# Kernel optimization log

Hardware: AMD Instinct MI355X
Metric: run time of the kernel (lower is better)

The kernel has to match this reference:

```python
import jax, jax.numpy as jnp
import numpy as np
from jax import lax

B, R, F = 100, 15, 4096       # batch, regions, feature dim
V, E, D, A, T = 10000, 1024, 1024, 512, 500  # vocab, embed, decoder, attention, topic
LIN = 1024                    # autoencoder linear output width
NT = 5                        # sentences per paragraph
L = 52                        # max caption length


def setup_inputs() -> dict:
    key = jax.random.key(0)
    ks = jax.random.split(key, 16)
    g = lambda i, shp, s: jax.random.normal(ks[i], shp, jnp.float32) * s
    return {
        "image_features": g(0, (B, R, F), 1.0),
        "encoded_captions": jax.random.randint(ks[1], (B, NT, L), 0, V),
        "caption_lengths": jax.random.randint(ks[2], (B, NT), 1, L),
        # autoencoder
        "W_lt": g(3, (LIN, F), 0.02), "b_lt": jnp.zeros((LIN,), jnp.float32),
        "conv_w": g(4, (6, 1, 15, 26), 0.05), "conv_b": jnp.zeros((6,), jnp.float32),
        # attention MLP (weight_norm linears == plain linears mathematically)
        "W_feat": g(5, (A, F), 0.02), "b_feat": jnp.zeros((A,), jnp.float32),
        "W_dec": g(6, (A, D), 0.02), "b_dec": jnp.zeros((A,), jnp.float32),
        "W_top": g(7, (A, T), 0.02), "b_top": jnp.zeros((A,), jnp.float32),
        "W_full": g(8, (1, A), 0.02), "b_full": jnp.zeros((1,), jnp.float32),
        # embedding + LSTM cells + output heads
        "emb": g(9, (V, E), 0.1),
        "W_ih1": g(10, (4 * D, E + F + D), 0.01), "W_hh1": g(11, (4 * D, D), 0.01),
        "b_ih1": jnp.zeros((4 * D,), jnp.float32), "b_hh1": jnp.zeros((4 * D,), jnp.float32),
        "W_ih2": g(12, (4 * D, F + D), 0.01), "W_hh2": g(13, (4 * D, D), 0.01),
        "b_ih2": jnp.zeros((4 * D,), jnp.float32), "b_hh2": jnp.zeros((4 * D,), jnp.float32),
        "W_fc1": g(14, (V, D), 0.02), "b_fc1": jnp.zeros((V,), jnp.float32),
        "W_fc": g(15, (V, D), 0.02), "b_fc": jnp.zeros((V,), jnp.float32),
    }


def _lstm_cell(x, h, c, W_ih, W_hh, b_ih, b_hh):
    gates = x @ W_ih.T + b_ih + h @ W_hh.T + b_hh
    i, f, g_, o = jnp.split(gates, 4, axis=-1)
    c = jax.nn.sigmoid(f) * c + jax.nn.sigmoid(i) * jnp.tanh(g_)
    h = jax.nn.sigmoid(o) * jnp.tanh(c)
    return h, c


def reference(image_features, encoded_captions, caption_lengths, W_lt, b_lt,
              conv_w, conv_b, W_feat, b_feat, W_dec, b_dec, W_top, b_top,
              W_full, b_full, emb, W_ih1, W_hh1, b_ih1, b_hh1,
              W_ih2, W_hh2, b_ih2, b_hh2, W_fc1, b_fc1, W_fc, b_fc):
    def per_sample(img, caps, lens):
        # img (R,F), caps (NT,L) int, lens (NT,) int
        img_mean = img.mean(0)  # (F,)
        # autoencoder: linear 4096->1024, conv2d(1->6, k=(15,26), stride 2)
        x = (img @ W_lt.T + b_lt)[None, None]  # (1,1,R,LIN)
        conv = lax.conv_general_dilated(x, conv_w, (2, 2), "VALID",
                                        dimension_numbers=("NCHW", "OIHW", "NCHW"))
        topics = conv[0, :, 0, :] + conv_b[:, None]  # (6, T=500)
        att1 = img @ W_feat.T + b_feat               # (R,A), precomputed once
        # last word of each sentence: caps[t, lens[t]-1]
        last_words = jnp.take_along_axis(caps, (lens - 1)[:, None], axis=1)[:, 0]  # (NT,)
        last_embs = emb[last_words]                  # (NT,E)

        def step(carry, tup):
            h1, c1, h2, c2 = carry
            topic_t, emb_t = tup
            # top-down attention LSTM: cat([h2, img_mean, word_emb])
            x1 = jnp.concatenate([h2, img_mean, emb_t])
            h1, c1 = _lstm_cell(x1, h1, c1, W_ih1, W_hh1, b_ih1, b_hh1)
            # attention over R regions (dropout is identity in eval)
            att = jax.nn.relu(att1 + (h1 @ W_dec.T + b_dec) + (topic_t @ W_top.T + b_top))
            scores = att @ W_full[0] + b_full[0]     # (R,)
            alpha = jax.nn.softmax(scores)
            awe = alpha @ img                        # (F,)
            preds1 = h1 @ W_fc1.T + b_fc1            # (V,)
            h2, c2 = _lstm_cell(jnp.concatenate([awe, h1]), h2, c2,
                                W_ih2, W_hh2, b_ih2, b_hh2)
            preds = h2 @ W_fc.T + b_fc               # (V,)
            return (h1, c1, h2, c2), (preds, preds1)

        z = jnp.zeros((D,), img.dtype)
        _, (preds, preds1) = lax.scan(step, (z, z, z, z), (topics[:NT], last_embs))
        return preds, preds1                          # (NT,V) each

    preds, preds1 = jax.vmap(per_sample)(image_features, encoded_captions, caption_lengths)
    return preds, preds1, encoded_captions, caption_lengths - 1
```

## Files before the change

### kernel.cpp

```cpp
#include <hip/hip_runtime.h>

typedef __attribute__((ext_vector_type(8))) short short8;
typedef __attribute__((ext_vector_type(4))) short short4v;
typedef __attribute__((ext_vector_type(4))) float f32x4;

__device__ __forceinline__ unsigned short f2bf(float f) {
  unsigned int u = __float_as_uint(f);
  u += 0x7fffu + ((u >> 16) & 1u);
  return (unsigned short)(u >> 16);
}
__device__ __forceinline__ float bf2f(unsigned short u) {
  return __uint_as_float(((unsigned int)u) << 16);
}
__device__ __forceinline__ float sigm(float x) { return 1.f / (1.f + expf(-x)); }

template<int NKC>
__global__ __launch_bounds__(256) void gemm_v5(
    const unsigned short* __restrict__ X, int ldx,
    const unsigned short* __restrict__ W, int ldw, int N,
    unsigned short* __restrict__ C, long long slotStride)
{
  __shared__ short8 lds[3584];
  const int tid = threadIdx.x;
  const int lane = tid & 63, wv = tid >> 6;
  const int l16 = lane & 15, kg = (lane >> 4) * 8;
  const int mbase = blockIdx.y * 112;
  const int ncol = blockIdx.x * 64 + wv * 16 + l16;
  const int nrow = (ncol < N) ? ncol : (N - 1);
  const long long k0 = (long long)blockIdx.z * (NKC * 256);
  C += (long long)blockIdx.z * slotStride;

  const unsigned short* wp = W + (size_t)nrow * ldw + kg + k0;
  const unsigned short* xb = X + (size_t)(mbase + l16) * ldx + kg + k0;
  const size_t xrow = (size_t)16 * ldx;

  f32x4 acc[7];
#pragma unroll
  for (int i = 0; i < 7; ++i) acc[i] = (f32x4){0.f, 0.f, 0.f, 0.f};

  for (int kc = 0; kc < NKC; ++kc) {
    if (kc) __syncthreads();
    short8 wbuf[8];
#pragma unroll
    for (int ks = 0; ks < 8; ++ks)
      wbuf[ks] = *(const short8*)(wp + kc * 256 + ks * 32);
    short8 xst[14];
#pragma unroll
    for (int i = 0; i < 14; ++i) {
      const int f = wv + i * 4, mt = f >> 3, ks = f & 7;
      xst[i] = *(const short8*)(xb + (size_t)mt * xrow + kc * 256 + ks * 32);
    }
#pragma unroll
    for (int i = 0; i < 14; ++i) lds[(wv + i * 4) * 64 + lane] = xst[i];
    __syncthreads();
#pragma unroll
    for (int ks = 0; ks < 8; ++ks)
#pragma unroll
      for (int mt = 0; mt < 7; ++mt) {
        short8 a = lds[(mt * 8 + ks) * 64 + lane];
        acc[mt] = __builtin_amdgcn_mfma_f32_16x16x32_bf16(a, wbuf[ks], acc[mt], 0, 0, 0);
      }
  }
  if (ncol < N) {
    const int r0 = (lane >> 4) * 4;
#pragma unroll
    for (int mt = 0; mt < 7; ++mt)
#pragma unroll
      for (int r = 0; r < 4; ++r)
        C[(size_t)(mbase + mt * 16 + r0 + r) * N + ncol] = f2bf(acc[mt][r]);
  }
}

template<int NKC>
__global__ __launch_bounds__(256) void gemm_v5f(
    const unsigned short* __restrict__ X, int ldx,
    const float* __restrict__ W, int ldw, int N,
    unsigned short* __restrict__ C, long long slotStride)
{
  __shared__ short8 lds[3584];
  const int tid = threadIdx.x;
  const int lane = tid & 63, wv = tid >> 6;
  const int l16 = lane & 15, kg = (lane >> 4) * 8;
  const int mbase = blockIdx.y * 112;
  const int ncol = blockIdx.x * 64 + wv * 16 + l16;
  const int nrow = (ncol < N) ? ncol : (N - 1);
  const long long k0 = (long long)blockIdx.z * (NKC * 256);
  C += (long long)blockIdx.z * slotStride;

  const float* wp = W + (size_t)nrow * ldw + kg + k0;
  const unsigned short* xb = X + (size_t)(mbase + l16) * ldx + kg + k0;
  const size_t xrow = (size_t)16 * ldx;

  f32x4 acc[7];
#pragma unroll
  for (int i = 0; i < 7; ++i) acc[i] = (f32x4){0.f, 0.f, 0.f, 0.f};

  for (int kc = 0; kc < NKC; ++kc) {
    if (kc) __syncthreads();
    float4 wa[8], wb[8];
#pragma unroll
    for (int ks = 0; ks < 8; ++ks) {
      wa[ks] = *(const float4*)(wp + kc * 256 + ks * 32);
      wb[ks] = *(const float4*)(wp + kc * 256 + ks * 32 + 4);
    }
    short8 xst[14];
#pragma unroll
    for (int i = 0; i < 14; ++i) {
      const int f = wv + i * 4, mt = f >> 3, ks = f & 7;
      xst[i] = *(const short8*)(xb + (size_t)mt * xrow + kc * 256 + ks * 32);
    }
#pragma unroll
    for (int i = 0; i < 14; ++i) lds[(wv + i * 4) * 64 + lane] = xst[i];
    __syncthreads();
#pragma unroll
    for (int ks = 0; ks < 8; ++ks) {
      short8 w;
      w[0] = (short)f2bf(wa[ks].x); w[1] = (short)f2bf(wa[ks].y);
      w[2] = (short)f2bf(wa[ks].z); w[3] = (short)f2bf(wa[ks].w);
      w[4] = (short)f2bf(wb[ks].x); w[5] = (short)f2bf(wb[ks].y);
      w[6] = (short)f2bf(wb[ks].z); w[7] = (short)f2bf(wb[ks].w);
#pragma unroll
      for (int mt = 0; mt < 7; ++mt) {
        short8 a = lds[(mt * 8 + ks) * 64 + lane];
        acc[mt] = __builtin_amdgcn_mfma_f32_16x16x32_bf16(a, w, acc[mt], 0, 0, 0);
      }
    }
  }
  if (ncol < N) {
    const int r0 = (lane >> 4) * 4;
#pragma unroll
    for (int mt = 0; mt < 7; ++mt)
#pragma unroll
      for (int r = 0; r < 4; ++r)
        C[(size_t)(mbase + mt * 16 + r0 + r) * N + ncol] = f2bf(acc[mt][r]);
  }
}

__global__ __launch_bounds__(256) void k_cvt4(const float* __restrict__ src,
                                              unsigned short* __restrict__ dst, int n4) {
  int i = blockIdx.x * 256 + threadIdx.x;
  if (i >= n4) return;
  float4 v = ((const float4*)src)[i];
  short4v o; o[0] = (short)f2bf(v.x); o[1] = (short)f2bf(v.y);
  o[2] = (short)f2bf(v.z); o[3] = (short)f2bf(v.w);
  ((short4v*)dst)[i] = o;
}

__global__ __launch_bounds__(256) void k_pack_g1(const float* __restrict__ Wih1,
    const float* __restrict__ Whh1, unsigned short* __restrict__ Wg1) {
  int i = blockIdx.x * 256 + threadIdx.x;
  if (i >= 4096 * 512) return;
  int row = i >> 9, c4 = i & 511;
  const float* src = (c4 < 256) ? Wih1 + (size_t)row * 6144 + c4 * 4
                                : Whh1 + (size_t)row * 1024 + (c4 - 256) * 4;
  float4 v = *(const float4*)src;
  short4v o; o[0] = (short)f2bf(v.x); o[1] = (short)f2bf(v.y);
  o[2] = (short)f2bf(v.z); o[3] = (short)f2bf(v.w);
  ((short4v*)Wg1)[i] = o;
}

__global__ __launch_bounds__(256) void k_pack_g2(const float* __restrict__ Wih2,
    const float* __restrict__ Whh2, unsigned short* __restrict__ Wg2) {
  int i = blockIdx.x * 256 + threadIdx.x;
  if (i >= 4096 * 1536) return;
  int row = i / 1536, c4 = i - row * 1536;
  const float* src = (c4 < 1280) ? Wih2 + (size_t)row * 5120 + c4 * 4
                                 : Whh2 + (size_t)row * 1024 + (c4 - 1280) * 4;
  float4 v = *(const float4*)src;
  short4v o; o[0] = (short)f2bf(v.x); o[1] = (short)f2bf(v.y);
  o[2] = (short)f2bf(v.z); o[3] = (short)f2bf(v.w);
  ((short4v*)Wg2)[i] = o;
}

__global__ __launch_bounds__(256) void k_ximg(const float* __restrict__ src,
                                              unsigned short* __restrict__ dst) {
  int idx = blockIdx.x * 256 + threadIdx.x;
  int row = idx >> 12;
  dst[idx] = (row < 1500) ? f2bf(src[idx]) : (unsigned short)0;
}

__global__ __launch_bounds__(256) void k_mean(const float* __restrict__ img,
                                              unsigned short* __restrict__ dst) {
  int idx = blockIdx.x * 256 + threadIdx.x;
  int b = idx >> 12, f = idx & 4095;
  unsigned short r = 0;
  if (b < 100) {
    float s = 0.f;
    for (int rr = 0; rr < 15; ++rr) s += img[((size_t)b * 15 + rr) * 4096 + f];
    r = f2bf(s * (1.f / 15.f));
  }
  dst[idx] = r;
}

__global__ __launch_bounds__(256) void k_reduce(const unsigned short* __restrict__ P,
    long long ss, int nslots, const float* __restrict__ bias, int colmask,
    float* __restrict__ out, int total) {
  int idx = blockIdx.x * 256 + threadIdx.x;
  if (idx >= total) return;
  float s = bias ? bias[idx & colmask] : 0.f;
  for (int sl = 0; sl < nslots; ++sl) s += bf2f(P[(size_t)sl * ss + idx]);
  out[idx] = s;
}

__global__ __launch_bounds__(512) void k_conv(const float* __restrict__ lin,
    const float* __restrict__ cw, const float* __restrict__ cb,
    float* __restrict__ topics) {
  int b = blockIdx.x;
  __shared__ float L[15 * 1024];
  for (int i = threadIdx.x; i < 15 * 1024; i += 512) L[i] = lin[(size_t)b * 15360 + i];
  __syncthreads();
  for (int idx = threadIdx.x; idx < 2500; idx += 512) {
    int tt = idx / 500, w = idx - tt * 500;
    float s = cb[tt];
    for (int kh = 0; kh < 15; ++kh) {
      const float* lr = &L[kh * 1024 + 2 * w];
      const float* wr = &cw[(tt * 15 + kh) * 26];
#pragma unroll
      for (int kw = 0; kw < 26; ++kw) s += lr[kw] * wr[kw];
    }
    topics[(size_t)b * 2500 + idx] = s;
  }
}

__global__ __launch_bounds__(256) void k_ttop(const float* __restrict__ topics,
    const float* __restrict__ Wt, const float* __restrict__ btp,
    float* __restrict__ ttop) {
  int idx = blockIdx.x * 256 + threadIdx.x;
  int r = idx >> 9, n = idx & 511;
  const float4* tr = (const float4*)(topics + (size_t)r * 500);
  const float4* wr = (const float4*)(Wt + (size_t)n * 500);
  float s = btp[n];
  for (int k = 0; k < 125; ++k) {
    float4 a = tr[k], w = wr[k];
    s += a.x * w.x + a.y * w.y + a.z * w.z + a.w * w.w;
  }
  ttop[idx] = s;
}

__global__ void k_words(const int* __restrict__ caps, const int* __restrict__ lens,
                        int* __restrict__ words, float* __restrict__ out3) {
  int idx = blockIdx.x * 256 + threadIdx.x;
  if (idx >= 500) return;
  int len = lens[idx];
  words[idx] = caps[idx * 52 + len - 1];
  out3[idx] = (float)(len - 1);
}

__global__ void k_caps(const int* __restrict__ caps, float* __restrict__ out2) {
  int idx = blockIdx.x * 256 + threadIdx.x;
  if (idx < 26000) out2[idx] = (float)caps[idx];
}

__global__ __launch_bounds__(256) void k_gather(const float* __restrict__ emb,
    const int* __restrict__ words, unsigned short* __restrict__ Xemb) {
  int idx = blockIdx.x * 256 + threadIdx.x;
  int bt = idx >> 10, e = idx & 1023;
  Xemb[idx] = (bt < 500) ? f2bf(emb[(size_t)words[bt] * 1024 + e]) : (unsigned short)0;
}

__global__ __launch_bounds__(256) void k_gbase1(const unsigned short* __restrict__ P,
    const float* __restrict__ bih, const float* __restrict__ bhh,
    float* __restrict__ gb) {
  int idx = blockIdx.x * 256 + threadIdx.x;
  int m = idx >> 12, n = idx & 4095;
  float s = bih[n] + bhh[n];
#pragma unroll
  for (int sl = 0; sl < 8; ++sl) s += bf2f(P[((size_t)sl * 112 + m) * 4096 + n]);
  gb[idx] = s;
}

__global__ __launch_bounds__(256) void k_lstm1(const unsigned short* __restrict__ P,
    const float* __restrict__ gb1, const float* __restrict__ gemb, int t,
    float* __restrict__ c1, unsigned short* __restrict__ Xh1,
    unsigned short* __restrict__ X1, unsigned short* __restrict__ X2) {
  int idx = blockIdx.x * 256 + threadIdx.x;
  int b = idx >> 10, j = idx & 1023;
  float g[4];
#pragma unroll
  for (int x = 0; x < 4; ++x) {
    int col = (x << 10) + j;
    float s = gb1[b * 4096 + col] + gemb[((size_t)b * 5 + t) * 4096 + col];
#pragma unroll
    for (int sl = 0; sl < 8; ++sl) s += bf2f(P[((size_t)sl * 112 + b) * 4096 + col]);
    g[x] = s;
  }
  float c = sigm(g[1]) * c1[idx] + sigm(g[0]) * tanhf(g[2]);
  float h = sigm(g[3]) * tanhf(c);
  c1[idx] = c;
  unsigned short hb = f2bf(h);
  Xh1[idx] = hb;
  X1[b * 2048 + 1024 + j] = hb;
  X2[(size_t)b * 6144 + 4096 + j] = hb;
}

__global__ __launch_bounds__(256) void k_att(const float* __restrict__ att1,
    const unsigned short* __restrict__ padec, const float* __restrict__ bdec,
    const float* __restrict__ ttop, const float* __restrict__ wfull,
    const float* __restrict__ bfull, int t, float* __restrict__ scores) {
  int wid = (blockIdx.x * 256 + threadIdx.x) >> 6;
  int lane = threadIdx.x & 63;
  if (wid >= 1500) return;
  int b = wid / 15;
  const float* a1 = att1 + (size_t)wid * 512;
  const float* tp = ttop + ((size_t)b * 5 + t) * 512;
  float s = 0.f;
#pragma unroll
  for (int j = 0; j < 8; ++j) {
    int n = lane * 8 + j;
    float ad = bdec[n] + bf2f(padec[(size_t)b * 512 + n])
             + bf2f(padec[(size_t)(112 + b) * 512 + n])
             + bf2f(padec[(size_t)(224 + b) * 512 + n])
             + bf2f(padec[(size_t)(336 + b) * 512 + n]);
    float v = a1[n] + ad + tp[n];
    s += fmaxf(v, 0.f) * wfull[n];
  }
#pragma unroll
  for (int o = 32; o; o >>= 1) s += __shfl_down(s, o, 64);
  if (lane == 0) scores[wid] = s + bfull[0];
}

__global__ __launch_bounds__(256) void k_softawe(const float* __restrict__ scores,
    const unsigned short* __restrict__ Ximg, unsigned short* __restrict__ X2) {
  int b = blockIdx.x;
  __shared__ float al[16];
  if (threadIdx.x == 0) {
    float m = -1e30f;
    for (int r = 0; r < 15; ++r) m = fmaxf(m, scores[b * 15 + r]);
    float e[15]; float sum = 0.f;
    for (int r = 0; r < 15; ++r) { e[r] = expf(scores[b * 15 + r] - m); sum += e[r]; }
    float inv = 1.f / sum;
    for (int r = 0; r < 15; ++r) al[r] = e[r] * inv;
  }
  __syncthreads();
  for (int f = threadIdx.x; f < 4096; f += 256) {
    float s = 0.f;
#pragma unroll
    for (int r = 0; r < 15; ++r) s += al[r] * bf2f(Ximg[((size_t)b * 15 + r) * 4096 + f]);
    X2[(size_t)b * 6144 + f] = f2bf(s);
  }
}

__global__ __launch_bounds__(256) void k_lstm2(const unsigned short* __restrict__ P,
    const float* __restrict__ bih, const float* __restrict__ bhh,
    float* __restrict__ c2, unsigned short* __restrict__ Xh2,
    unsigned short* __restrict__ X1, unsigned short* __restrict__ X2) {
  int idx = blockIdx.x * 256 + threadIdx.x;
  int b = idx >> 10, j = idx & 1023;
  float g[4];
#pragma unroll
  for (int x = 0; x < 4; ++x) {
    int col = (x << 10) + j;
    float s = bih[col] + bhh[col];
#pragma unroll
    for (int sl = 0; sl < 12; ++sl) s += bf2f(P[((size_t)sl * 112 + b) * 4096 + col]);
    g[x] = s;
  }
  float c = sigm(g[1]) * c2[idx] + sigm(g[0]) * tanhf(g[2]);
  float h = sigm(g[3]) * tanhf(c);
  c2[idx] = c;
  unsigned short hb = f2bf(h);
  Xh2[idx] = hb;
  X1[b * 2048 + j] = hb;
  X2[(size_t)b * 6144 + 5120 + j] = hb;
}

__global__ __launch_bounds__(256) void k_eppred(const unsigned short* __restrict__ P,
    const float* __restrict__ bias, float* __restrict__ outp, int t) {
  int idx = blockIdx.x * 256 + threadIdx.x;
  if (idx >= 1000000) return;
  int b = idx / 10000, v = idx - b * 10000;
  outp[((size_t)b * 5 + t) * 10000 + v] = bias[v]
      + bf2f(P[(size_t)b * 10000 + v])         + bf2f(P[(size_t)(112 + b) * 10000 + v])
      + bf2f(P[(size_t)(224 + b) * 10000 + v]) + bf2f(P[(size_t)(336 + b) * 10000 + v]);
}

extern "C" void kernel_launch(void* const* d_in, const int* in_sizes, int n_in,
                              void* d_out, int out_size, void* d_ws, size_t ws_size,
                              hipStream_t stream) {
  (void)in_sizes; (void)n_in; (void)out_size;
  const float* imgf  = (const float*)d_in[0];
  const int*   caps  = (const int*)d_in[1];
  const int*   lens  = (const int*)d_in[2];
  const float* W_lt  = (const float*)d_in[3];
  const float* b_lt  = (const float*)d_in[4];
  const float* convw = (const float*)d_in[5];
  const float* convb = (const float*)d_in[6];
  const float* W_feat = (const float*)d_in[7];
  const float* b_feat = (const float*)d_in[8];
  const float* W_dec = (const float*)d_in[9];
  const float* b_dec = (const float*)d_in[10];
  const float* W_top = (const float*)d_in[11];
  const float* b_top = (const float*)d_in[12];
  const float* W_full = (const float*)d_in[13];
  const float* b_full = (const float*)d_in[14];
  const float* emb   = (const float*)d_in[15];
  const float* W_ih1 = (const float*)d_in[16];
  const float* W_hh1 = (const float*)d_in[17];
  const float* b_ih1 = (const float*)d_in[18];
  const float* b_hh1 = (const float*)d_in[19];
  const float* W_ih2 = (const float*)d_in[20];
  const float* W_hh2 = (const float*)d_in[21];
  const float* b_ih2 = (const float*)d_in[22];
  const float* b_hh2 = (const float*)d_in[23];
  const float* W_fc1 = (const float*)d_in[24];
  const float* b_fc1 = (const float*)d_in[25];
  const float* W_fc  = (const float*)d_in[26];
  const float* b_fc  = (const float*)d_in[27];
  float* out = (float*)d_out;

  char* ws = (char*)d_ws;
  size_t off = 0;
  auto alloc = [&](size_t bytes) -> size_t {
    size_t o = off; off = (off + bytes + 255) & ~(size_t)255; return o;
  };
  const size_t oXimg  = alloc(1568ull * 4096 * 2);
  const size_t oXmean = alloc(112ull * 4096 * 2);
  const size_t oXemb  = alloc(560ull * 1024 * 2);
  const size_t oZERO  = off;
  const size_t oX1    = alloc(112ull * 2048 * 2);
  const size_t oX2    = alloc(112ull * 6144 * 2);
  const size_t oXh1   = alloc(112ull * 1024 * 2);
  const size_t oXh2   = alloc(112ull * 1024 * 2);
  const size_t oc1    = alloc(100ull * 1024 * 4);
  const size_t oc2    = alloc(100ull * 1024 * 4);
  const size_t zeroBytes = off - oZERO;
  const size_t olin   = alloc(1568ull * 1024 * 4);
  const size_t otop   = alloc(100ull * 2500 * 4);
  const size_t ottop  = alloc(500ull * 512 * 4);
  const size_t oatt1  = alloc(1568ull * 512 * 4);
  const size_t oscore = alloc(1536ull * 4);
  const size_t ogb1   = alloc(112ull * 4096 * 4);
  const size_t ogemb  = alloc(560ull * 4096 * 4);
  const size_t owords = alloc(512ull * 4);
  const size_t opg    = alloc(12ull * 112 * 4096 * 2);
  const size_t opx    = alloc(4ull * 1568 * 1024 * 2);
  const size_t oWg1   = alloc(4096ull * 2048 * 2);
  const size_t oWg2   = alloc(4096ull * 6144 * 2);
  const size_t oWfc1b = alloc(10000ull * 1024 * 2);
  const size_t oWfcb  = alloc(10000ull * 1024 * 2);
  const size_t oWdecb = alloc(512ull * 1024 * 2);
  const size_t oWltb  = alloc(1024ull * 4096 * 2);
  const size_t oWftb  = alloc(512ull * 4096 * 2);
  if (ws_size < off) return;

  unsigned short* Ximg  = (unsigned short*)(ws + oXimg);
  unsigned short* Xmean = (unsigned short*)(ws + oXmean);
  unsigned short* Xemb  = (unsigned short*)(ws + oXemb);
  unsigned short* X1    = (unsigned short*)(ws + oX1);
  unsigned short* X2    = (unsigned short*)(ws + oX2);
  unsigned short* Xh1   = (unsigned short*)(ws + oXh1);
  unsigned short* Xh2   = (unsigned short*)(ws + oXh2);
  float* c1    = (float*)(ws + oc1);
  float* c2    = (float*)(ws + oc2);
  float* lin   = (float*)(ws + olin);
  float* topics = (float*)(ws + otop);
  float* ttop  = (float*)(ws + ottop);
  float* att1  = (float*)(ws + oatt1);
  float* score = (float*)(ws + oscore);
  float* gb1   = (float*)(ws + ogb1);
  float* gemb  = (float*)(ws + ogemb);
  int*   words = (int*)(ws + owords);
  unsigned short* pg = (unsigned short*)(ws + opg);
  unsigned short* px = (unsigned short*)(ws + opx);
  unsigned short* Wg1   = (unsigned short*)(ws + oWg1);
  unsigned short* Wg2   = (unsigned short*)(ws + oWg2);
  unsigned short* Wfc1b = (unsigned short*)(ws + oWfc1b);
  unsigned short* Wfcb  = (unsigned short*)(ws + oWfcb);
  unsigned short* Wdecb = (unsigned short*)(ws + oWdecb);
  unsigned short* Wltb  = (unsigned short*)(ws + oWltb);
  unsigned short* Wftb  = (unsigned short*)(ws + oWftb);

  const long long S4 = 112ll * 4096;
  const long long SA = 112ll * 512;
  const long long SP = 112ll * 10000;

  hipMemsetAsync(ws + oZERO, 0, zeroBytes, stream);

  k_ximg<<<25088, 256, 0, stream>>>(imgf, Ximg);
  k_mean<<<1792, 256, 0, stream>>>(imgf, Xmean);
  k_pack_g1<<<8192, 256, 0, stream>>>(W_ih1, W_hh1, Wg1);
  k_pack_g2<<<24576, 256, 0, stream>>>(W_ih2, W_hh2, Wg2);
  k_cvt4<<<10000, 256, 0, stream>>>(W_fc1, Wfc1b, 2560000);
  k_cvt4<<<10000, 256, 0, stream>>>(W_fc, Wfcb, 2560000);
  k_cvt4<<<512, 256, 0, stream>>>(W_dec, Wdecb, 131072);
  k_cvt4<<<4096, 256, 0, stream>>>(W_lt, Wltb, 1048576);
  k_cvt4<<<2048, 256, 0, stream>>>(W_feat, Wftb, 524288);
  gemm_v5<4><<<dim3(16, 14, 4), 256, 0, stream>>>(Ximg, 4096, Wltb, 4096, 1024,
                                                  px, 1568ll * 1024);
  k_reduce<<<6272, 256, 0, stream>>>(px, 1568ll * 1024, 4, b_lt, 1023, lin, 1568 * 1024);
  k_conv<<<100, 512, 0, stream>>>(lin, convw, convb, topics);
  k_ttop<<<1000, 256, 0, stream>>>(topics, W_top, b_top, ttop);
  gemm_v5<4><<<dim3(8, 14, 4), 256, 0, stream>>>(Ximg, 4096, Wftb, 4096, 512,
                                                 px, 1568ll * 512);
  k_reduce<<<3136, 256, 0, stream>>>(px, 1568ll * 512, 4, b_feat, 511, att1, 1568 * 512);
  k_words<<<2, 256, 0, stream>>>(caps, lens, words, out + 10026000);
  k_caps<<<102, 256, 0, stream>>>(caps, out + 10000000);
  k_gather<<<2240, 256, 0, stream>>>(emb, words, Xemb);
  gemm_v5f<2><<<dim3(64, 1, 8), 256, 0, stream>>>(Xmean, 4096, W_ih1 + 1024, 6144, 4096,
                                                  pg, S4);
  k_gbase1<<<1792, 256, 0, stream>>>(pg, b_ih1, b_hh1, gb1);
  gemm_v5f<1><<<dim3(64, 5, 4), 256, 0, stream>>>(Xemb, 1024, W_ih1 + 5120, 6144, 4096,
                                                  px, 560ll * 4096);
  k_reduce<<<8960, 256, 0, stream>>>(px, 560ll * 4096, 4, nullptr, 4095, gemb, 560 * 4096);

  for (int t = 0; t < 5; ++t) {
    gemm_v5<1><<<dim3(64, 1, 8), 256, 0, stream>>>(X1, 2048, Wg1, 2048, 4096, pg, S4);
    k_lstm1<<<400, 256, 0, stream>>>(pg, gb1, gemb, t, c1, Xh1, X1, X2);
    gemm_v5<1><<<dim3(8, 1, 4), 256, 0, stream>>>(Xh1, 1024, Wdecb, 1024, 512, px, SA);
    k_att<<<375, 256, 0, stream>>>(att1, px, b_dec, ttop, W_full, b_full, t, score);
    k_softawe<<<100, 256, 0, stream>>>(score, Ximg, X2);
    gemm_v5<1><<<dim3(157, 1, 4), 256, 0, stream>>>(Xh1, 1024, Wfc1b, 1024, 10000, px, SP);
    k_eppred<<<3907, 256, 0, stream>>>(px, b_fc1, out + 5000000, t);
    gemm_v5<2><<<dim3(64, 1, 12), 256, 0, stream>>>(X2, 6144, Wg2, 6144, 4096, pg, S4);
    k_lstm2<<<400, 256, 0, stream>>>(pg, b_ih2, b_hh2, c2, Xh2, X1, X2);
    gemm_v5<1><<<dim3(157, 1, 4), 256, 0, stream>>>(Xh2, 1024, Wfcb, 1024, 10000, px, SP);
    k_eppred<<<3907, 256, 0, stream>>>(px, b_fc, out, t);
  }
}
```

Measured before the change: 789.7 us.

## Fuse weight packing, attention, and fc1/dec GEMMs; reduce launch count

Result: faster. 704.5 us (-10.8%).

```diff
diff --git a/kernel.cpp b/kernel.cpp
--- a/kernel.cpp
+++ b/kernel.cpp
@@ -136,40 +136,46 @@
   }
 }
 
-__global__ __launch_bounds__(256) void k_cvt4(const float* __restrict__ src,
-                                              unsigned short* __restrict__ dst, int n4) {
+__global__ __launch_bounds__(256) void k_pack_all(
+    const float* __restrict__ Wih1, const float* __restrict__ Whh1,
+    const float* __restrict__ Wih2, const float* __restrict__ Whh2,
+    const float* __restrict__ Wfc1, const float* __restrict__ Wdec,
+    const float* __restrict__ Wfc,  const float* __restrict__ Wlt,
+    const float* __restrict__ Wft,  const float* __restrict__ Wtop,
+    unsigned short* __restrict__ Wg1, unsigned short* __restrict__ Wg2,
+    unsigned short* __restrict__ Wcat, unsigned short* __restrict__ Wfcb,
+    unsigned short* __restrict__ Wltb, unsigned short* __restrict__ Wftb,
+    unsigned short* __restrict__ Wtopb)
+{
   int i = blockIdx.x * 256 + threadIdx.x;
-  if (i >= n4) return;
-  float4 v = ((const float4*)src)[i];
+  float4 v; unsigned short* dst; long long di;
+  if (i < 2097152) {
+    int row = i >> 9, c4 = i & 511;
+    const float* s = (c4 < 256) ? Wih1 + (size_t)row * 6144 + c4 * 4
+                                : Whh1 + (size_t)row * 1024 + (c4 - 256) * 4;
+    v = *(const float4*)s; dst = Wg1; di = i;
+  } else if (i < 8388608) {
+    int j = i - 2097152; int row = j / 1536, c4 = j - row * 1536;
+    const float* s = (c4 < 1280) ? Wih2 + (size_t)row * 5120 + c4 * 4
+                                 : Whh2 + (size_t)row * 1024 + (c4 - 1280) * 4;
+    v = *(const float4*)s; dst = Wg2; di = j;
+  } else if (i < 11079680) {
+    int j = i - 8388608; int row = j >> 8, c4 = j & 255;
+    const float* s = (row < 10000) ? Wfc1 + (size_t)row * 1024 + c4 * 4
+                                   : Wdec + (size_t)(row - 10000) * 1024 + c4 * 4;
+    v = *(const float4*)s; dst = Wcat; di = j;
+  } else if (i < 13639680) { int j = i - 11079680; v = ((const float4*)Wfc)[j]; dst = Wfcb; di = j; }
+  else if (i < 14688256) { int j = i - 13639680; v = ((const float4*)Wlt)[j]; dst = Wltb; di = j; }
+  else if (i < 15212544) { int j = i - 14688256; v = ((const float4*)Wft)[j]; dst = Wftb; di = j; }
+  else {
+    int j = i - 15212544; int n = j >> 7, c4 = j & 127;
+    v = (c4 < 125) ? *(const float4*)(Wtop + (size_t)n * 500 + c4 * 4)
+                   : (float4){0.f, 0.f, 0.f, 0.f};
+    dst = Wtopb; di = j;
+  }
   short4v o; o[0] = (short)f2bf(v.x); o[1] = (short)f2bf(v.y);
   o[2] = (short)f2bf(v.z); o[3] = (short)f2bf(v.w);
-  ((short4v*)dst)[i] = o;
-}
-
-__global__ __launch_bounds__(256) void k_pack_g1(const float* __restrict__ Wih1,
-    const float* __restrict__ Whh1, unsigned short* __restrict__ Wg1) {
-  int i = blockIdx.x * 256 + threadIdx.x;
-  if (i >= 4096 * 512) return;
-  int row = i >> 9, c4 = i & 511;
-  const float* src = (c4 < 256) ? Wih1 + (size_t)row * 6144 + c4 * 4
-                                : Whh1 + (size_t)row * 1024 + (c4 - 256) * 4;
-  float4 v = *(const float4*)src;
-  short4v o; o[0] = (short)f2bf(v.x); o[1] = (short)f2bf(v.y);
-  o[2] = (short)f2bf(v.z); o[3] = (short)f2bf(v.w);
-  ((short4v*)Wg1)[i] = o;
-}
-
-__global__ __launch_bounds__(256) void k_pack_g2(const float* __restrict__ Wih2,
-    const float* __restrict__ Whh2, unsigned short* __restrict__ Wg2) {
-  int i = blockIdx.x * 256 + threadIdx.x;
-  if (i >= 4096 * 1536) return;
-  int row = i / 1536, c4 = i - row * 1536;
-  const float* src = (c4 < 1280) ? Wih2 + (size_t)row * 5120 + c4 * 4
-                                 : Whh2 + (size_t)row * 1024 + (c4 - 1280) * 4;
-  float4 v = *(const float4*)src;
-  short4v o; o[0] = (short)f2bf(v.x); o[1] = (short)f2bf(v.y);
-  o[2] = (short)f2bf(v.z); o[3] = (short)f2bf(v.w);
-  ((short4v*)Wg2)[i] = o;
+  ((short4v*)dst)[di] = o;
 }
 
 __global__ __launch_bounds__(256) void k_ximg(const float* __restrict__ src,
@@ -202,12 +208,18 @@
   out[idx] = s;
 }
 
-__global__ __launch_bounds__(512) void k_conv(const float* __restrict__ lin,
-    const float* __restrict__ cw, const float* __restrict__ cb,
-    float* __restrict__ topics) {
+__global__ __launch_bounds__(512) void k_conv(const unsigned short* __restrict__ px,
+    const float* __restrict__ blt, const float* __restrict__ cw,
+    const float* __restrict__ cb, float* __restrict__ topics) {
   int b = blockIdx.x;
   __shared__ float L[15 * 1024];
-  for (int i = threadIdx.x; i < 15 * 1024; i += 512) L[i] = lin[(size_t)b * 15360 + i];
+  for (int i = threadIdx.x; i < 15 * 1024; i += 512) {
+    float s = blt[i & 1023];
+#pragma unroll
+    for (int sl = 0; sl < 4; ++sl)
+      s += bf2f(px[(size_t)sl * 1605632 + (size_t)b * 15360 + i]);
+    L[i] = s;
+  }
   __syncthreads();
   for (int idx = threadIdx.x; idx < 2500; idx += 512) {
     int tt = idx / 500, w = idx - tt * 500;
@@ -222,33 +234,24 @@
   }
 }
 
-__global__ __launch_bounds__(256) void k_ttop(const float* __restrict__ topics,
-    const float* __restrict__ Wt, const float* __restrict__ btp,
-    float* __restrict__ ttop) {
-  int idx = blockIdx.x * 256 + threadIdx.x;
-  int r = idx >> 9, n = idx & 511;
-  const float4* tr = (const float4*)(topics + (size_t)r * 500);
-  const float4* wr = (const float4*)(Wt + (size_t)n * 500);
-  float s = btp[n];
-  for (int k = 0; k < 125; ++k) {
-    float4 a = tr[k], w = wr[k];
-    s += a.x * w.x + a.y * w.y + a.z * w.z + a.w * w.w;
-  }
-  ttop[idx] = s;
-}
-
-__global__ void k_words(const int* __restrict__ caps, const int* __restrict__ lens,
-                        int* __restrict__ words, float* __restrict__ out3) {
-  int idx = blockIdx.x * 256 + threadIdx.x;
-  if (idx >= 500) return;
-  int len = lens[idx];
-  words[idx] = caps[idx * 52 + len - 1];
-  out3[idx] = (float)(len - 1);
-}
-
-__global__ void k_caps(const int* __restrict__ caps, float* __restrict__ out2) {
+__global__ __launch_bounds__(256) void k_padtop(const float* __restrict__ topics,
+    unsigned short* __restrict__ Xtop) {
+  int idx = blockIdx.x * 256 + threadIdx.x;
+  if (idx >= 560 * 512) return;
+  int r = idx >> 9, k = idx & 511;
+  Xtop[idx] = (r < 500 && k < 500) ? f2bf(topics[(size_t)r * 500 + k]) : (unsigned short)0;
+}
+
+__global__ void k_wc(const int* __restrict__ caps, const int* __restrict__ lens,
+                     int* __restrict__ words, float* __restrict__ out2,
+                     float* __restrict__ out3) {
   int idx = blockIdx.x * 256 + threadIdx.x;
   if (idx < 26000) out2[idx] = (float)caps[idx];
+  if (idx < 500) {
+    int len = lens[idx];
+    words[idx] = caps[idx * 52 + len - 1];
+    out3[idx] = (float)(len - 1);
+  }
 }
 
 __global__ __launch_bounds__(256) void k_gather(const float* __restrict__ emb,
@@ -293,50 +296,54 @@
   X2[(size_t)b * 6144 + 4096 + j] = hb;
 }
 
-__global__ __launch_bounds__(256) void k_att(const float* __restrict__ att1,
+__global__ __launch_bounds__(256) void k_attawe(const float* __restrict__ att1,
     const unsigned short* __restrict__ padec, const float* __restrict__ bdec,
-    const float* __restrict__ ttop, const float* __restrict__ wfull,
-    const float* __restrict__ bfull, int t, float* __restrict__ scores) {
-  int wid = (blockIdx.x * 256 + threadIdx.x) >> 6;
-  int lane = threadIdx.x & 63;
-  if (wid >= 1500) return;
-  int b = wid / 15;
-  const float* a1 = att1 + (size_t)wid * 512;
-  const float* tp = ttop + ((size_t)b * 5 + t) * 512;
-  float s = 0.f;
-#pragma unroll
-  for (int j = 0; j < 8; ++j) {
-    int n = lane * 8 + j;
-    float ad = bdec[n] + bf2f(padec[(size_t)b * 512 + n])
-             + bf2f(padec[(size_t)(112 + b) * 512 + n])
-             + bf2f(padec[(size_t)(224 + b) * 512 + n])
-             + bf2f(padec[(size_t)(336 + b) * 512 + n]);
-    float v = a1[n] + ad + tp[n];
-    s += fmaxf(v, 0.f) * wfull[n];
-  }
-#pragma unroll
-  for (int o = 32; o; o >>= 1) s += __shfl_down(s, o, 64);
-  if (lane == 0) scores[wid] = s + bfull[0];
-}
-
-__global__ __launch_bounds__(256) void k_softawe(const float* __restrict__ scores,
+    const float* __restrict__ btop, const unsigned short* __restrict__ ttopb,
+    const float* __restrict__ wfull, int t,
     const unsigned short* __restrict__ Ximg, unsigned short* __restrict__ X2) {
   int b = blockIdx.x;
+  int tid = threadIdx.x;
+  int r = tid & 15, ch = tid >> 4;
+  __shared__ float sp[16][17];
   __shared__ float al[16];
-  if (threadIdx.x == 0) {
+  float s = 0.f;
+  if (r < 15) {
+    const float* a1 = att1 + ((size_t)b * 15 + r) * 512;
+    const unsigned short* tp = ttopb + ((size_t)b * 5 + t) * 512;
+#pragma unroll
+    for (int j = 0; j < 32; ++j) {
+      int n = ch * 32 + j;
+      float ad = bdec[n] + btop[n]
+               + bf2f(padec[((size_t)0 * 112 + b) * 10512 + 10000 + n])
+               + bf2f(padec[((size_t)1 * 112 + b) * 10512 + 10000 + n])
+               + bf2f(padec[((size_t)2 * 112 + b) * 10512 + 10000 + n])
+               + bf2f(padec[((size_t)3 * 112 + b) * 10512 + 10000 + n]);
+      float v = a1[n] + ad + bf2f(tp[n]);
+      s += fmaxf(v, 0.f) * wfull[n];
+    }
+  }
+  sp[r][ch] = s;
+  __syncthreads();
+  if (tid == 0) {
+    float sc[15];
     float m = -1e30f;
-    for (int r = 0; r < 15; ++r) m = fmaxf(m, scores[b * 15 + r]);
-    float e[15]; float sum = 0.f;
-    for (int r = 0; r < 15; ++r) { e[r] = expf(scores[b * 15 + r] - m); sum += e[r]; }
+    for (int rr = 0; rr < 15; ++rr) {
+      float x = 0.f;
+      for (int cc = 0; cc < 16; ++cc) x += sp[rr][cc];
+      sc[rr] = x; m = fmaxf(m, x);
+    }
+    float sum = 0.f;
+    for (int rr = 0; rr < 15; ++rr) { sc[rr] = expf(sc[rr] - m); sum += sc[rr]; }
     float inv = 1.f / sum;
-    for (int r = 0; r < 15; ++r) al[r] = e[r] * inv;
+    for (int rr = 0; rr < 15; ++rr) al[rr] = sc[rr] * inv;
   }
   __syncthreads();
-  for (int f = threadIdx.x; f < 4096; f += 256) {
-    float s = 0.f;
-#pragma unroll
-    for (int r = 0; r < 15; ++r) s += al[r] * bf2f(Ximg[((size_t)b * 15 + r) * 4096 + f]);
-    X2[(size_t)b * 6144 + f] = f2bf(s);
+  for (int f = tid; f < 4096; f += 256) {
+    float s2 = 0.f;
+#pragma unroll
+    for (int rr = 0; rr < 15; ++rr)
+      s2 += al[rr] * bf2f(Ximg[((size_t)b * 15 + rr) * 4096 + f]);
+    X2[(size_t)b * 6144 + f] = f2bf(s2);
   }
 }
 
@@ -365,13 +372,13 @@
 }
 
 __global__ __launch_bounds__(256) void k_eppred(const unsigned short* __restrict__ P,
-    const float* __restrict__ bias, float* __restrict__ outp, int t) {
+    const float* __restrict__ bias, float* __restrict__ outp, int t, int ldp) {
   int idx = blockIdx.x * 256 + threadIdx.x;
   if (idx >= 1000000) return;
   int b = idx / 10000, v = idx - b * 10000;
   outp[((size_t)b * 5 + t) * 10000 + v] = bias[v]
-      + bf2f(P[(size_t)b * 10000 + v])         + bf2f(P[(size_t)(112 + b) * 10000 + v])
-      + bf2f(P[(size_t)(224 + b) * 10000 + v]) + bf2f(P[(size_t)(336 + b) * 10000 + v]);
+      + bf2f(P[(size_t)(0 * 112 + b) * ldp + v]) + bf2f(P[(size_t)(112 + b) * ldp + v])
+      + bf2f(P[(size_t)(224 + b) * ldp + v])     + bf2f(P[(size_t)(336 + b) * ldp + v]);
 }
 
 extern "C" void kernel_launch(void* const* d_in, const int* in_sizes, int n_in,
@@ -392,7 +399,7 @@
   const float* W_top = (const float*)d_in[11];
   const float* b_top = (const float*)d_in[12];
   const float* W_full = (const float*)d_in[13];
-  const float* b_full = (const float*)d_in[14];
+  const float* b_full = (const float*)d_in[14];  (void)b_full;
   const float* emb   = (const float*)d_in[15];
   const float* W_ih1 = (const float*)d_in[16];
   const float* W_hh1 = (const float*)d_in[17];
@@ -424,23 +431,22 @@
   const size_t oc1    = alloc(100ull * 1024 * 4);
   const size_t oc2    = alloc(100ull * 1024 * 4);
   const size_t zeroBytes = off - oZERO;
-  const size_t olin   = alloc(1568ull * 1024 * 4);
   const size_t otop   = alloc(100ull * 2500 * 4);
-  const size_t ottop  = alloc(500ull * 512 * 4);
+  const size_t oXtop  = alloc(560ull * 512 * 2);
+  const size_t oTtopb = alloc(560ull * 512 * 2);
   const size_t oatt1  = alloc(1568ull * 512 * 4);
-  const size_t oscore = alloc(1536ull * 4);
   const size_t ogb1   = alloc(112ull * 4096 * 4);
   const size_t ogemb  = alloc(560ull * 4096 * 4);
   const size_t owords = alloc(512ull * 4);
   const size_t opg    = alloc(12ull * 112 * 4096 * 2);
-  const size_t opx    = alloc(4ull * 1568 * 1024 * 2);
+  const size_t opx    = alloc(4ull * 560 * 4096 * 2);
   const size_t oWg1   = alloc(4096ull * 2048 * 2);
   const size_t oWg2   = alloc(4096ull * 6144 * 2);
-  const size_t oWfc1b = alloc(10000ull * 1024 * 2);
+  const size_t oWcat  = alloc(10512ull * 1024 * 2);
   const size_t oWfcb  = alloc(10000ull * 1024 * 2);
-  const size_t oWdecb = alloc(512ull * 1024 * 2);
   const size_t oWltb  = alloc(1024ull * 4096 * 2);
   const size_t oWftb  = alloc(512ull * 4096 * 2);
+  const size_t oWtopb = alloc(512ull * 512 * 2);
   if (ws_size < off) return;
 
   unsigned short* Ximg  = (unsigned short*)(ws + oXimg);
@@ -452,11 +458,10 @@
   unsigned short* Xh2   = (unsigned short*)(ws + oXh2);
   float* c1    = (float*)(ws + oc1);
   float* c2    = (float*)(ws + oc2);
-  float* lin   = (float*)(ws + olin);
   float* topics = (float*)(ws + otop);
-  float* ttop  = (float*)(ws + ottop);
+  unsigned short* Xtop  = (unsigned short*)(ws + oXtop);
+  unsigned short* Ttopb = (unsigned short*)(ws + oTtopb);
   float* att1  = (float*)(ws + oatt1);
-  float* score = (float*)(ws + oscore);
   float* gb1   = (float*)(ws + ogb1);
   float* gemb  = (float*)(ws + ogemb);
   int*   words = (int*)(ws + owords);
@@ -464,37 +469,32 @@
   unsigned short* px = (unsigned short*)(ws + opx);
   unsigned short* Wg1   = (unsigned short*)(ws + oWg1);
   unsigned short* Wg2   = (unsigned short*)(ws + oWg2);
-  unsigned short* Wfc1b = (unsigned short*)(ws + oWfc1b);
+  unsigned short* Wcat  = (unsigned short*)(ws + oWcat);
   unsigned short* Wfcb  = (unsigned short*)(ws + oWfcb);
-  unsigned short* Wdecb = (unsigned short*)(ws + oWdecb);
   unsigned short* Wltb  = (unsigned short*)(ws + oWltb);
   unsigned short* Wftb  = (unsigned short*)(ws + oWftb);
-
-  const long long S4 = 112ll * 4096;
-  const long long SA = 112ll * 512;
-  const long long SP = 112ll * 10000;
+  unsigned short* Wtopb = (unsigned short*)(ws + oWtopb);
+
+  const long long S4  = 112ll * 4096;
+  const long long SP1 = 112ll * 10512;
+  const long long SP  = 112ll * 10000;
 
   hipMemsetAsync(ws + oZERO, 0, zeroBytes, stream);
 
   k_ximg<<<25088, 256, 0, stream>>>(imgf, Ximg);
   k_mean<<<1792, 256, 0, stream>>>(imgf, Xmean);
-  k_pack_g1<<<8192, 256, 0, stream>>>(W_ih1, W_hh1, Wg1);
-  k_pack_g2<<<24576, 256, 0, stream>>>(W_ih2, W_hh2, Wg2);
-  k_cvt4<<<10000, 256, 0, stream>>>(W_fc1, Wfc1b, 2560000);
-  k_cvt4<<<10000, 256, 0, stream>>>(W_fc, Wfcb, 2560000);
-  k_cvt4<<<512, 256, 0, stream>>>(W_dec, Wdecb, 131072);
-  k_cvt4<<<4096, 256, 0, stream>>>(W_lt, Wltb, 1048576);
-  k_cvt4<<<2048, 256, 0, stream>>>(W_feat, Wftb, 524288);
+  k_pack_all<<<59680, 256, 0, stream>>>(W_ih1, W_hh1, W_ih2, W_hh2, W_fc1, W_dec,
+                                        W_fc, W_lt, W_feat, W_top,
+                                        Wg1, Wg2, Wcat, Wfcb, Wltb, Wftb, Wtopb);
   gemm_v5<4><<<dim3(16, 14, 4), 256, 0, stream>>>(Ximg, 4096, Wltb, 4096, 1024,
                                                   px, 1568ll * 1024);
-  k_reduce<<<6272, 256, 0, stream>>>(px, 1568ll * 1024, 4, b_lt, 1023, lin, 1568 * 1024);
-  k_conv<<<100, 512, 0, stream>>>(lin, convw, convb, topics);
-  k_ttop<<<1000, 256, 0, stream>>>(topics, W_top, b_top, ttop);
+  k_conv<<<100, 512, 0, stream>>>(px, b_lt, convw, convb, topics);
+  k_padtop<<<1120, 256, 0, stream>>>(topics, Xtop);
+  gemm_v5<2><<<dim3(8, 5, 1), 256, 0, stream>>>(Xtop, 512, Wtopb, 512, 512, Ttopb, 0);
   gemm_v5<4><<<dim3(8, 14, 4), 256, 0, stream>>>(Ximg, 4096, Wftb, 4096, 512,
                                                  px, 1568ll * 512);
   k_reduce<<<3136, 256, 0, stream>>>(px, 1568ll * 512, 4, b_feat, 511, att1, 1568 * 512);
-  k_words<<<2, 256, 0, stream>>>(caps, lens, words, out + 10026000);
-  k_caps<<<102, 256, 0, stream>>>(caps, out + 10000000);
+  k_wc<<<102, 256, 0, stream>>>(caps, lens, words, out + 10000000, out + 10026000);
   k_gather<<<2240, 256, 0, stream>>>(emb, words, Xemb);
   gemm_v5f<2><<<dim3(64, 1, 8), 256, 0, stream>>>(Xmean, 4096, W_ih1 + 1024, 6144, 4096,
                                                   pg, S4);
@@ -506,14 +506,12 @@
   for (int t = 0; t < 5; ++t) {
     gemm_v5<1><<<dim3(64, 1, 8), 256, 0, stream>>>(X1, 2048, Wg1, 2048, 4096, pg, S4);
     k_lstm1<<<400, 256, 0, stream>>>(pg, gb1, gemb, t, c1, Xh1, X1, X2);
-    gemm_v5<1><<<dim3(8, 1, 4), 256, 0, stream>>>(Xh1, 1024, Wdecb, 1024, 512, px, SA);
-    k_att<<<375, 256, 0, stream>>>(att1, px, b_dec, ttop, W_full, b_full, t, score);
-    k_softawe<<<100, 256, 0, stream>>>(score, Ximg, X2);
-    gemm_v5<1><<<dim3(157, 1, 4), 256, 0, stream>>>(Xh1, 1024, Wfc1b, 1024, 10000, px, SP);
-    k_eppred<<<3907, 256, 0, stream>>>(px, b_fc1, out + 5000000, t);
+    gemm_v5<1><<<dim3(165, 1, 4), 256, 0, stream>>>(Xh1, 1024, Wcat, 1024, 10512, px, SP1);
+    k_attawe<<<100, 256, 0, stream>>>(att1, px, b_dec, b_top, Ttopb, W_full, t, Ximg, X2);
+    k_eppred<<<3907, 256, 0, stream>>>(px, b_fc1, out + 5000000, t, 10512);
     gemm_v5<2><<<dim3(64, 1, 12), 256, 0, stream>>>(X2, 6144, Wg2, 6144, 4096, pg, S4);
     k_lstm2<<<400, 256, 0, stream>>>(pg, b_ih2, b_hh2, c2, Xh2, X1, X2);
     gemm_v5<1><<<dim3(157, 1, 4), 256, 0, stream>>>(Xh2, 1024, Wfcb, 1024, 10000, px, SP);
-    k_eppred<<<3907, 256, 0, stream>>>(px, b_fc, out, t);
-  }
-}
+    k_eppred<<<3907, 256, 0, stream>>>(px, b_fc, out, t, 10000);
+  }
+}
```
